# Performance work log

Measured on AMD Instinct MI355X. Metric: run time of the kernel, lower is better.

The kernel has to match this reference:

```python
import jax, jax.numpy as jnp
import numpy as np

DIM_DICT = 64
SIZE_DICT = 512
TEMPERATURE = 0.5
EPS_GUMBEL = 1e-10
EPS_NORM = 1e-12
EPS_PPL = 1e-7


def _l2_normalize(x, axis):
    # torch F.normalize: x / max(||x||, eps)
    n = jnp.sqrt(jnp.sum(x * x, axis=axis, keepdims=True))
    return x / jnp.maximum(n, EPS_NORM)


def setup_inputs() -> dict:
    key = jax.random.key(0)
    k1, k2, k3 = jax.random.split(key, 3)
    bs, seq_len, d = 8, 1024, 512
    z = jax.random.normal(k1, (bs, seq_len, d), dtype=jnp.float32)
    codebook = jax.random.normal(k2, (SIZE_DICT, DIM_DICT), dtype=jnp.float32)
    n_flat = bs * seq_len * (d // DIM_DICT)
    gumbel_u = jax.random.uniform(k3, (n_flat, SIZE_DICT), dtype=jnp.float32)
    kappa_q = jnp.float32(1.0)
    return {"z_from_encoder": z, "kappa_q": kappa_q, "codebook": codebook,
            "gumbel_u": gumbel_u}


def reference(z_from_encoder, kappa_q, codebook, gumbel_u):
    bs, seq_len, d = z_from_encoder.shape
    # [bs, seq, groups, dim_dict], L2-normalized along dim_dict
    z_perm = z_from_encoder.reshape(bs, seq_len, -1, DIM_DICT)
    z_norm = _l2_normalize(z_perm, axis=3)
    cb_norm = _l2_normalize(codebook, axis=1)  # [K, dim]

    # logit = -distance = kappa_q * <z, c>   -> [N, K]
    z_flat = z_norm.reshape(-1, DIM_DICT)
    logit = kappa_q * jnp.matmul(z_flat, cb_norm.T)

    log_probabilities = jax.nn.log_softmax(logit, axis=-1)
    probabilities = jnp.exp(log_probabilities)

    # gumbel-softmax sample (train path)
    g = -jnp.log(-jnp.log(gumbel_u + EPS_GUMBEL) + EPS_GUMBEL)
    encodings = jax.nn.softmax((logit + g) / TEMPERATURE, axis=-1)

    z_quantized = jnp.matmul(encodings, cb_norm).reshape(z_perm.shape)
    z_to_decoder = z_quantized.reshape(bs, seq_len, -1)

    avg_probs = jnp.mean(jax.lax.stop_gradient(probabilities), axis=0)  # [K]

    kld_discrete = jnp.sum(probabilities * log_probabilities) / bs
    kld_continuous = jnp.mean(
        jnp.sum(z_from_encoder * (z_from_encoder - z_to_decoder) * kappa_q,
                axis=(1, 2)))
    loss = kld_discrete + kld_continuous
    perplexity = jnp.exp(-jnp.sum(avg_probs * jnp.log(avg_probs + EPS_PPL)))
    return z_to_decoder, loss, perplexity
```

## Files before the change

### kernel.cpp

```cpp
#include <hip/hip_runtime.h>
#include <cstdint>
#include <cstddef>


typedef __attribute__((ext_vector_type(8))) short short8;
typedef __attribute__((ext_vector_type(4))) float f32x4;

namespace {
constexpr float kEpsG = 1e-10f;
constexpr float kEpsN = 1e-12f;
constexpr float kEpsP = 1e-7f;
constexpr float kLog2e = 1.4426950408889634f;
constexpr float kLn2 = 0.6931471805599453f;
constexpr int kSlots = 128;
constexpr int kStride = 520;
constexpr int kOffCbn = 0;
constexpr int kOffCbt = 65536;
constexpr int kOffAvg = 131072;
constexpr int kOffCS  = 139264;
constexpr int kOffAcx = 140800;
constexpr int kLdsBytes = 157184;
}

__device__ __forceinline__ float wsum64(float v) {
#pragma unroll
    for (int m = 1; m < 64; m <<= 1) v += __shfl_xor(v, m, 64);
    return v;
}
__device__ __forceinline__ uint32_t pk_bf16(float a, float b) {
    uint32_t ua = __float_as_uint(a), ub = __float_as_uint(b);
    ua += 0x7fffu + ((ua >> 16) & 1u);
    ub += 0x7fffu + ((ub >> 16) & 1u);
    return (ua >> 16) | (ub & 0xffff0000u);
}
__device__ __forceinline__ uint16_t bf16_rne(float a) {
    uint32_t ua = __float_as_uint(a);
    ua += 0x7fffu + ((ua >> 16) & 1u);
    return (uint16_t)(ua >> 16);
}
__device__ __forceinline__ float dot4(float4 v) {
    return v.x * v.x + v.y * v.y + v.z * v.z + v.w * v.w;
}

__global__ __launch_bounds__(256) void k_prep(const float* __restrict__ cb,
                                              uint16_t* __restrict__ cbN,
                                              uint16_t* __restrict__ cbNT) {
    const int row = blockIdx.x * 4 + (threadIdx.x >> 6);
    const int lane = threadIdx.x & 63;
    const float v = cb[row * 64 + lane];
    const float ss = wsum64(v * v);
    const float nv = v / fmaxf(sqrtf(ss), kEpsN);
    const uint16_t h = bf16_rne(nv);
    cbN[row * 64 + lane] = h;
    cbNT[lane * 512 + row] = h;
}

__global__ __launch_bounds__(512, 2) void k_main(
    const float* __restrict__ z, const float* __restrict__ kqp,
    const float* __restrict__ gum, const uint16_t* __restrict__ cbN,
    const uint16_t* __restrict__ cbNT, float* __restrict__ out,
    float* __restrict__ g_part) {
    extern __shared__ float4 smem_al[];
    char* smem = (char*)smem_al;
    float* avg4 = (float*)(smem + kOffAvg);
    float (*cS)[2][16]  = (float(*)[2][16])(smem + kOffCS);
    float (*cW)[2][16]  = (float(*)[2][16])(smem + kOffCS + 512);
    float (*cS2)[2][16] = (float(*)[2][16])(smem + kOffCS + 1024);
    float4 (*accx)[2][2][64] = (float4(*)[2][2][64])(smem + kOffAcx);

    const int tid = threadIdx.x;
    const int wv = tid >> 6;
    const int tp = wv >> 1;
    const int W = wv & 1;
    const int l = tid & 63;
    const int g = l >> 4;
    const int rh = l & 15;
    const int r0 = blockIdx.x * 64 + tp * 16;
    const int row = r0 + rh;
    const float kq = *kqp;

#pragma unroll
    for (int it = 0; it < 16; ++it) {
        const int i = tid + 512 * it;
        const uint4 v = ((const uint4*)cbN)[i];
        const int r = i >> 3, c = i & 7;
        *(uint4*)(smem + r * 128 + (((c ^ (r & 7))) << 4)) = v;
    }
#pragma unroll
    for (int it = 0; it < 8; ++it) {
        const int i = tid + 512 * it;
        const uint4 v = ((const uint4*)cbNT)[i];
        const int d = i >> 6, c = i & 63;
        *(uint4*)(smem + kOffCbt + d * 1024 + ((c ^ (d & 7)) << 4)) = v;
    }

    const float* zr = z + (size_t)row * 64;
    const float4 a0 = *(const float4*)(zr + 8 * g);
    const float4 a1 = *(const float4*)(zr + 8 * g + 4);
    const float4 a2 = *(const float4*)(zr + 32 + 8 * g);
    const float4 a3 = *(const float4*)(zr + 36 + 8 * g);
    float ss = dot4(a0) + dot4(a1) + dot4(a2) + dot4(a3);
    ss += __shfl_xor(ss, 16, 64);
    ss += __shfl_xor(ss, 32, 64);
    const float scz = kq * kLog2e / fmaxf(sqrtf(ss), kEpsN);
    union U8 { short8 s; uint32_t u[4]; };
    U8 zb0, zb1;
    zb0.u[0] = pk_bf16(a0.x * scz, a0.y * scz);
    zb0.u[1] = pk_bf16(a0.z * scz, a0.w * scz);
    zb0.u[2] = pk_bf16(a1.x * scz, a1.y * scz);
    zb0.u[3] = pk_bf16(a1.z * scz, a1.w * scz);
    zb1.u[0] = pk_bf16(a2.x * scz, a2.y * scz);
    zb1.u[1] = pk_bf16(a2.z * scz, a2.w * scz);
    zb1.u[2] = pk_bf16(a3.x * scz, a3.y * scz);
    zb1.u[3] = pk_bf16(a3.z * scz, a3.w * scz);

    const float B1 = kq * kLog2e;

    const float* ur = gum + (size_t)row * 512 + 256 * W;
    float4 uN[4][4];
#pragma unroll
    for (int t = 0; t < 4; ++t)
#pragma unroll
        for (int j = 0; j < 4; ++j)
            uN[t][j] = *(const float4*)(ur + 64 * t + 16 * j + 4 * g);

    __syncthreads();

    uint32_t epk[32];
    float S4[4] = {0.f, 0.f, 0.f, 0.f}, W4[4] = {0.f, 0.f, 0.f, 0.f};
#pragma unroll
    for (int T = 0; T < 4; ++T) {
#pragma unroll
        for (int q = 0; q < 4; ++q) {
            const int R = 256 * W + 64 * T + 16 * q + rh;
            const char* rb = smem + R * 128;
            const short8 ca0 = *(const short8*)(rb + ((g ^ (R & 7)) << 4));
            const short8 ca1 = *(const short8*)(rb + (((g + 4) ^ (R & 7)) << 4));
            f32x4 acc = {0.f, 0.f, 0.f, 0.f};
            acc = __builtin_amdgcn_mfma_f32_16x16x32_bf16(ca0, zb0.s, acc, 0, 0, 0);
            acc = __builtin_amdgcn_mfma_f32_16x16x32_bf16(ca1, zb1.s, acc, 0, 0, 0);
            float e4[4];
#pragma unroll
            for (int i = 0; i < 4; ++i) {
                const float d = acc[i] - B1;
                const float e = __builtin_amdgcn_exp2f(d);
                e4[i] = e;
                S4[i] += e;
                W4[i] = fmaf(d, e, W4[i]);
            }
            epk[8 * T + 2 * q] = pk_bf16(e4[0], e4[1]);
            epk[8 * T + 2 * q + 1] = pk_bf16(e4[2], e4[3]);
        }
    }
    float Sr = (S4[0] + S4[1]) + (S4[2] + S4[3]);
    float Wr = (W4[0] + W4[1]) + (W4[2] + W4[3]);
    Sr += __shfl_xor(Sr, 16, 64);
    Sr += __shfl_xor(Sr, 32, 64);
    Wr += __shfl_xor(Wr, 16, 64);
    Wr += __shfl_xor(Wr, 32, 64);
    if (g == 0) { cS[tp][W][rh] = Sr; cW[tp][W][rh] = Wr; }
    __syncthreads();
    const float St = cS[tp][0][rh] + cS[tp][1][rh];
    const float Wt = cW[tp][0][rh] + cW[tp][1][rh];
    const float inv = 1.0f / St;
    const float kldd = kLn2 * (Wt * inv - __builtin_amdgcn_logf(St));

    float S24[4] = {0.f, 0.f, 0.f, 0.f};
    f32x4 acc2[4];
#pragma unroll
    for (int dt = 0; dt < 4; ++dt) acc2[dt] = (f32x4){0.f, 0.f, 0.f, 0.f};
    const int srcA = rh + 16 * ((2 * g) & 3);
    const int srcB = rh + 16 * ((2 * g + 1) & 3);
    const bool hi = (g & 2) != 0;

#pragma unroll
    for (int T = 0; T < 4; ++T) {
        float ev[16];
#pragma unroll
        for (int k2 = 0; k2 < 8; ++k2) {
            const uint32_t pe = epk[8 * T + k2];
            ev[2 * k2] = __uint_as_float(pe << 16);
            ev[2 * k2 + 1] = __uint_as_float(pe & 0xffff0000u);
        }

        float pf[8];
#pragma unroll
        for (int q = 0; q < 4; ++q) {
            const float uu[4] = {uN[T][q].x, uN[T][q].y, uN[T][q].z, uN[T][q].w};
            float e2v[4];
#pragma unroll
            for (int i = 0; i < 4; ++i) {
                const float lg = __builtin_amdgcn_logf(uu[i] + kEpsG);
                const float inr = fmaf(lg, -kLn2, kEpsG);
                const float r = __builtin_amdgcn_rcpf(inr);
                const float t = ev[4 * q + i] * r;
                const float e2 = t * t;
                e2v[i] = e2;
                S24[i] += e2;
            }
            pf[2 * q] = __uint_as_float(pk_bf16(e2v[0], e2v[1]));
            pf[2 * q + 1] = __uint_as_float(pk_bf16(e2v[2], e2v[3]));
        }

#pragma unroll
        for (int j = 0; j < 16; ++j) ev[j] *= inv;
#pragma unroll
        for (int m = 1, nv = 8; m <= 8; m <<= 1, nv >>= 1) {
            const bool up_ = (rh & m) != 0;
#pragma unroll
            for (int t = 0; t < nv; ++t) {
                const float a = ev[t], b = ev[t + nv];
                const float keep = up_ ? b : a;
                const float send = up_ ? a : b;
                ev[t] = keep + __shfl_xor(send, m, 64);
            }
        }
        const int jr = ((rh & 1) << 3) | ((rh & 2) << 1) | ((rh & 4) >> 1) |
                       ((rh & 8) >> 3);
        avg4[tp * 512 + 256 * W + 64 * T + 16 * (jr >> 2) + 4 * g + (jr & 3)] =
            ev[0];

#pragma unroll
        for (int ks = 0; ks < 2; ++ks) {
            const float a0lo = __shfl(pf[4 * ks + 0], srcA, 64);
            const float a1lo = __shfl(pf[4 * ks + 1], srcA, 64);
            const float a0hi = __shfl(pf[4 * ks + 2], srcA, 64);
            const float a1hi = __shfl(pf[4 * ks + 3], srcA, 64);
            const float b0lo = __shfl(pf[4 * ks + 0], srcB, 64);
            const float b1lo = __shfl(pf[4 * ks + 1], srcB, 64);
            const float b0hi = __shfl(pf[4 * ks + 2], srcB, 64);
            const float b1hi = __shfl(pf[4 * ks + 3], srcB, 64);
            U8 af;
            af.u[0] = __float_as_uint(hi ? a0hi : a0lo);
            af.u[1] = __float_as_uint(hi ? a1hi : a1lo);
            af.u[2] = __float_as_uint(hi ? b0hi : b0lo);
            af.u[3] = __float_as_uint(hi ? b1hi : b1lo);
#pragma unroll
            for (int dt = 0; dt < 4; ++dt) {
                const int D = rh + 16 * dt;
                const int c = 32 * W + 8 * T + 4 * ks + g;
                const short8 bf = *(const short8*)(smem + kOffCbt + D * 1024 +
                                                   ((c ^ (D & 7)) << 4));
                acc2[dt] = __builtin_amdgcn_mfma_f32_16x16x32_bf16(
                    af.s, bf, acc2[dt], 0, 0, 0);
            }
        }
    }

    float S2r = (S24[0] + S24[1]) + (S24[2] + S24[3]);
    S2r += __shfl_xor(S2r, 16, 64);
    S2r += __shfl_xor(S2r, 32, 64);
    if (g == 0) cS2[tp][W][rh] = S2r;
    if (W == 0) {
        accx[tp][0][0][l] = make_float4(acc2[2][0], acc2[2][1], acc2[2][2], acc2[2][3]);
        accx[tp][0][1][l] = make_float4(acc2[3][0], acc2[3][1], acc2[3][2], acc2[3][3]);
    } else {
        accx[tp][1][0][l] = make_float4(acc2[0][0], acc2[0][1], acc2[0][2], acc2[0][3]);
        accx[tp][1][1][l] = make_float4(acc2[1][0], acc2[1][1], acc2[1][2], acc2[1][3]);
    }
    __syncthreads();
    const float inv2 = 1.0f / (cS2[tp][0][rh] + cS2[tp][1][rh]);
    float ivi[4];
#pragma unroll
    for (int i = 0; i < 4; ++i) ivi[i] = __shfl(inv2, 4 * g + i, 64);

    float kldc = 0.f;
#define EPI(OV, XV, DT)                                                       \
    {                                                                         \
        const float oq[4] = {OV[0] + XV.x, OV[1] + XV.y, OV[2] + XV.z,        \
                             OV[3] + XV.w};                                   \
        _Pragma("unroll") for (int i = 0; i < 4; ++i) {                       \
            const float q = oq[i] * ivi[i];                                   \
            const size_t oi = (size_t)(r0 + 4 * g + i) * 64 + rh + 16 * (DT); \
            out[oi] = q;                                                      \
            const float zv = z[oi];                                           \
            kldc = fmaf(zv, zv - q, kldc);                                    \
        }                                                                     \
    }
    if (W == 0) {
        const float4 x0 = accx[tp][1][0][l];
        const float4 x1 = accx[tp][1][1][l];
        EPI(acc2[0], x0, 0)
        EPI(acc2[1], x1, 1)
    } else {
        const float4 x0 = accx[tp][0][0][l];
        const float4 x1 = accx[tp][0][1][l];
        EPI(acc2[2], x0, 2)
        EPI(acc2[3], x1, 3)
    }

    const int slot = blockIdx.x & (kSlots - 1);
    float* gp = g_part + (size_t)slot * kStride;
    const float kc = wsum64(kldc) * kq;
    const float kd = wsum64(kldd) * 0.25f;
    if (l == 0) {
        atomicAdd(&gp[513], kc);
        if (W == 0) atomicAdd(&gp[512], kd);
    }
    const float av = avg4[tid] + avg4[512 + tid] + avg4[1024 + tid] +
                     avg4[1536 + tid];
    atomicAdd(&gp[tid], av);
}

__global__ __launch_bounds__(512) void k_final(const float* __restrict__ g_part,
                                               float* __restrict__ out) {
    __shared__ float red[8];
    const int tid = threadIdx.x;
    float sacc = 0.f;
#pragma unroll 8
    for (int i = 0; i < kSlots; ++i) sacc += g_part[(size_t)i * kStride + tid];
    const float avg = sacc * (1.0f / 65536.0f);
    const float t = avg * __logf(avg + kEpsP);
    const float sw = wsum64(t);
    if ((tid & 63) == 0) red[tid >> 6] = sw;
    __syncthreads();
    if (tid == 0) {
        float tot = 0.f;
#pragma unroll
        for (int i = 0; i < 8; ++i) tot += red[i];
        float sc0 = 0.f, sc1 = 0.f;
        for (int i = 0; i < kSlots; ++i) {
            sc0 += g_part[(size_t)i * kStride + 512];
            sc1 += g_part[(size_t)i * kStride + 513];
        }
        out[4194304] = (sc0 + sc1) * 0.125f;
        out[4194305] = __expf(-tot);
    }
}

extern "C" void kernel_launch(void* const* d_in, const int* in_sizes, int n_in,
                              void* d_out, int out_size, void* d_ws, size_t ws_size,
                              hipStream_t stream) {
    (void)in_sizes; (void)n_in; (void)out_size; (void)ws_size;
    const float* z   = (const float*)d_in[0];
    const float* kq  = (const float*)d_in[1];
    const float* cb  = (const float*)d_in[2];
    const float* gum = (const float*)d_in[3];
    float* out = (float*)d_out;

    uint16_t* cbN  = (uint16_t*)d_ws;
    uint16_t* cbNT = cbN + 32768;
    float* g_part  = (float*)(cbNT + 32768);

    (void)hipFuncSetAttribute((const void*)k_main,
                              hipFuncAttributeMaxDynamicSharedMemorySize,
                              kLdsBytes);
    (void)hipMemsetAsync(g_part, 0, kSlots * kStride * sizeof(float), stream);
    k_prep<<<128, 256, 0, stream>>>(cb, cbN, cbNT);
    k_main<<<1024, 512, kLdsBytes, stream>>>(z, kq, gum, cbN, cbNT, out, g_part);
    k_final<<<1, 512, 0, stream>>>(g_part, out);
}
```

Measured before the change: 86.63 us.

## Fuse gumbel softmax and second matmul into logit tile loop with double-buffered loads

The gumbel-weighted exponentials and the encodings×codebook MFMA accumulation move into the same per-tile loop that computes the logits, so they no longer wait for a separate second pass. The uniform-noise loads now use two four-float4 buffers that are refilled two tiles ahead, replacing one 16-register array. This should cut register pressure and let global loads and transcendental math overlap with MFMA work. It relies on the unnormalized exp (e, not e/St) feeding the gumbel weights, which the original already did, and it keeps the averaging pass separate.

```diff
diff --git a/kernel.cpp b/kernel.cpp
--- a/kernel.cpp
+++ b/kernel.cpp
@@ -14,7 +14,6 @@
 constexpr float kLn2 = 0.6931471805599453f;
 constexpr int kSlots = 128;
 constexpr int kStride = 520;
-constexpr int kOffCbn = 0;
 constexpr int kOffCbt = 65536;
 constexpr int kOffAvg = 131072;
 constexpr int kOffCS  = 139264;
@@ -117,41 +116,95 @@
     const float B1 = kq * kLog2e;
 
     const float* ur = gum + (size_t)row * 512 + 256 * W;
-    float4 uN[4][4];
-#pragma unroll
-    for (int t = 0; t < 4; ++t)
-#pragma unroll
-        for (int j = 0; j < 4; ++j)
-            uN[t][j] = *(const float4*)(ur + 64 * t + 16 * j + 4 * g);
+    float4 uA[4], uB[4];
+#pragma unroll
+    for (int j = 0; j < 4; ++j) uA[j] = *(const float4*)(ur + 16 * j + 4 * g);
+#pragma unroll
+    for (int j = 0; j < 4; ++j)
+        uB[j] = *(const float4*)(ur + 64 + 16 * j + 4 * g);
 
     __syncthreads();
 
     uint32_t epk[32];
     float S4[4] = {0.f, 0.f, 0.f, 0.f}, W4[4] = {0.f, 0.f, 0.f, 0.f};
-#pragma unroll
-    for (int T = 0; T < 4; ++T) {
-#pragma unroll
-        for (int q = 0; q < 4; ++q) {
-            const int R = 256 * W + 64 * T + 16 * q + rh;
-            const char* rb = smem + R * 128;
-            const short8 ca0 = *(const short8*)(rb + ((g ^ (R & 7)) << 4));
-            const short8 ca1 = *(const short8*)(rb + (((g + 4) ^ (R & 7)) << 4));
-            f32x4 acc = {0.f, 0.f, 0.f, 0.f};
-            acc = __builtin_amdgcn_mfma_f32_16x16x32_bf16(ca0, zb0.s, acc, 0, 0, 0);
-            acc = __builtin_amdgcn_mfma_f32_16x16x32_bf16(ca1, zb1.s, acc, 0, 0, 0);
-            float e4[4];
-#pragma unroll
-            for (int i = 0; i < 4; ++i) {
-                const float d = acc[i] - B1;
-                const float e = __builtin_amdgcn_exp2f(d);
-                e4[i] = e;
-                S4[i] += e;
-                W4[i] = fmaf(d, e, W4[i]);
-            }
-            epk[8 * T + 2 * q] = pk_bf16(e4[0], e4[1]);
-            epk[8 * T + 2 * q + 1] = pk_bf16(e4[2], e4[3]);
-        }
-    }
+    float S24[4] = {0.f, 0.f, 0.f, 0.f};
+    f32x4 acc2[4];
+#pragma unroll
+    for (int dt = 0; dt < 4; ++dt) acc2[dt] = (f32x4){0.f, 0.f, 0.f, 0.f};
+    const int srcA = rh + 16 * ((2 * g) & 3);
+    const int srcB = rh + 16 * ((2 * g + 1) & 3);
+    const bool hi = (g & 2) != 0;
+
+#define RELOAD(UB, RT)                                                       \
+    _Pragma("unroll") for (int j = 0; j < 4; ++j)                            \
+        UB[j] = *(const float4*)(ur + 64 * (RT) + 16 * j + 4 * g);
+
+#define FTILE(T, UBUF, PRE)                                                  \
+    {                                                                        \
+        float pf[8];                                                         \
+        _Pragma("unroll") for (int q = 0; q < 4; ++q) {                      \
+            const int R = 256 * W + 64 * (T) + 16 * q + rh;                  \
+            const char* rb = smem + R * 128;                                 \
+            const short8 ca0 = *(const short8*)(rb + ((g ^ (R & 7)) << 4));  \
+            const short8 ca1 =                                               \
+                *(const short8*)(rb + (((g + 4) ^ (R & 7)) << 4));           \
+            f32x4 acc = {0.f, 0.f, 0.f, 0.f};                                \
+            acc = __builtin_amdgcn_mfma_f32_16x16x32_bf16(ca0, zb0.s, acc,   \
+                                                          0, 0, 0);          \
+            acc = __builtin_amdgcn_mfma_f32_16x16x32_bf16(ca1, zb1.s, acc,   \
+                                                          0, 0, 0);          \
+            const float uu[4] = {UBUF[q].x, UBUF[q].y, UBUF[q].z, UBUF[q].w};\
+            float e4[4], e2v[4];                                             \
+            _Pragma("unroll") for (int i = 0; i < 4; ++i) {                  \
+                const float d = acc[i] - B1;                                 \
+                const float e = __builtin_amdgcn_exp2f(d);                   \
+                e4[i] = e;                                                   \
+                S4[i] += e;                                                  \
+                W4[i] = fmaf(d, e, W4[i]);                                   \
+                const float lg = __builtin_amdgcn_logf(uu[i] + kEpsG);       \
+                const float inr = fmaf(lg, -kLn2, kEpsG);                    \
+                const float r = __builtin_amdgcn_rcpf(inr);                  \
+                const float t = e * r;                                       \
+                const float e2 = t * t;                                      \
+                e2v[i] = e2;                                                 \
+                S24[i] += e2;                                                \
+            }                                                                \
+            epk[8 * (T) + 2 * q] = pk_bf16(e4[0], e4[1]);                    \
+            epk[8 * (T) + 2 * q + 1] = pk_bf16(e4[2], e4[3]);                \
+            pf[2 * q] = __uint_as_float(pk_bf16(e2v[0], e2v[1]));            \
+            pf[2 * q + 1] = __uint_as_float(pk_bf16(e2v[2], e2v[3]));        \
+        }                                                                    \
+        PRE                                                                  \
+        _Pragma("unroll") for (int ks = 0; ks < 2; ++ks) {                   \
+            const float a0lo = __shfl(pf[4 * ks + 0], srcA, 64);             \
+            const float a1lo = __shfl(pf[4 * ks + 1], srcA, 64);             \
+            const float a0hi = __shfl(pf[4 * ks + 2], srcA, 64);             \
+            const float a1hi = __shfl(pf[4 * ks + 3], srcA, 64);             \
+            const float b0lo = __shfl(pf[4 * ks + 0], srcB, 64);             \
+            const float b1lo = __shfl(pf[4 * ks + 1], srcB, 64);             \
+            const float b0hi = __shfl(pf[4 * ks + 2], srcB, 64);             \
+            const float b1hi = __shfl(pf[4 * ks + 3], srcB, 64);             \
+            U8 af;                                                           \
+            af.u[0] = __float_as_uint(hi ? a0hi : a0lo);                     \
+            af.u[1] = __float_as_uint(hi ? a1hi : a1lo);                     \
+            af.u[2] = __float_as_uint(hi ? b0hi : b0lo);                     \
+            af.u[3] = __float_as_uint(hi ? b1hi : b1lo);                     \
+            _Pragma("unroll") for (int dt = 0; dt < 4; ++dt) {               \
+                const int D = rh + 16 * dt;                                  \
+                const int c = 32 * W + 8 * (T) + 4 * ks + g;                 \
+                const short8 bf = *(const short8*)(smem + kOffCbt +          \
+                    D * 1024 + ((c ^ (D & 7)) << 4));                        \
+                acc2[dt] = __builtin_amdgcn_mfma_f32_16x16x32_bf16(          \
+                    af.s, bf, acc2[dt], 0, 0, 0);                            \
+            }                                                                \
+        }                                                                    \
+    }
+
+    FTILE(0, uA, RELOAD(uA, 2))
+    FTILE(1, uB, RELOAD(uB, 3))
+    FTILE(2, uA, ;)
+    FTILE(3, uB, ;)
+
     float Sr = (S4[0] + S4[1]) + (S4[2] + S4[3]);
     float Wr = (W4[0] + W4[1]) + (W4[2] + W4[3]);
     Sr += __shfl_xor(Sr, 16, 64);
@@ -165,14 +218,6 @@
     const float inv = 1.0f / St;
     const float kldd = kLn2 * (Wt * inv - __builtin_amdgcn_logf(St));
 
-    float S24[4] = {0.f, 0.f, 0.f, 0.f};
-    f32x4 acc2[4];
-#pragma unroll
-    for (int dt = 0; dt < 4; ++dt) acc2[dt] = (f32x4){0.f, 0.f, 0.f, 0.f};
-    const int srcA = rh + 16 * ((2 * g) & 3);
-    const int srcB = rh + 16 * ((2 * g + 1) & 3);
-    const bool hi = (g & 2) != 0;
-
 #pragma unroll
     for (int T = 0; T < 4; ++T) {
         float ev[16];
@@ -182,26 +227,6 @@
             ev[2 * k2] = __uint_as_float(pe << 16);
             ev[2 * k2 + 1] = __uint_as_float(pe & 0xffff0000u);
         }
-
-        float pf[8];
-#pragma unroll
-        for (int q = 0; q < 4; ++q) {
-            const float uu[4] = {uN[T][q].x, uN[T][q].y, uN[T][q].z, uN[T][q].w};
-            float e2v[4];
-#pragma unroll
-            for (int i = 0; i < 4; ++i) {
-                const float lg = __builtin_amdgcn_logf(uu[i] + kEpsG);
-                const float inr = fmaf(lg, -kLn2, kEpsG);
-                const float r = __builtin_amdgcn_rcpf(inr);
-                const float t = ev[4 * q + i] * r;
-                const float e2 = t * t;
-                e2v[i] = e2;
-                S24[i] += e2;
-            }
-            pf[2 * q] = __uint_as_float(pk_bf16(e2v[0], e2v[1]));
-            pf[2 * q + 1] = __uint_as_float(pk_bf16(e2v[2], e2v[3]));
-        }
-
 #pragma unroll
         for (int j = 0; j < 16; ++j) ev[j] *= inv;
 #pragma unroll
@@ -219,32 +244,6 @@
                        ((rh & 8) >> 3);
         avg4[tp * 512 + 256 * W + 64 * T + 16 * (jr >> 2) + 4 * g + (jr & 3)] =
             ev[0];
-
-#pragma unroll
-        for (int ks = 0; ks < 2; ++ks) {
-            const float a0lo = __shfl(pf[4 * ks + 0], srcA, 64);
-            const float a1lo = __shfl(pf[4 * ks + 1], srcA, 64);
-            const float a0hi = __shfl(pf[4 * ks + 2], srcA, 64);
-            const float a1hi = __shfl(pf[4 * ks + 3], srcA, 64);
-            const float b0lo = __shfl(pf[4 * ks + 0], srcB, 64);
-            const float b1lo = __shfl(pf[4 * ks + 1], srcB, 64);
-            const float b0hi = __shfl(pf[4 * ks + 2], srcB, 64);
-            const float b1hi = __shfl(pf[4 * ks + 3], srcB, 64);
-            U8 af;
-            af.u[0] = __float_as_uint(hi ? a0hi : a0lo);
-            af.u[1] = __float_as_uint(hi ? a1hi : a1lo);
-            af.u[2] = __float_as_uint(hi ? b0hi : b0lo);
-            af.u[3] = __float_as_uint(hi ? b1hi : b1lo);
-#pragma unroll
-            for (int dt = 0; dt < 4; ++dt) {
-                const int D = rh + 16 * dt;
-                const int c = 32 * W + 8 * T + 4 * ks + g;
-                const short8 bf = *(const short8*)(smem + kOffCbt + D * 1024 +
-                                                   ((c ^ (D & 7)) << 4));
-                acc2[dt] = __builtin_amdgcn_mfma_f32_16x16x32_bf16(
-                    af.s, bf, acc2[dt], 0, 0, 0);
-            }
-        }
     }
 
     float S2r = (S24[0] + S24[1]) + (S24[2] + S24[3]);
```

Measured after the change: 84.76 us. 1.02x faster.

## Use 1024-thread blocks, recompute logits to drop stored exponentials, LDS atomic avg

Applied to the files above, without the earlier changes.

Each block now covers 128 rows with 1024 threads, so the 128 KB codebook LDS fill is amortized over twice as many rows and half as many blocks load it. The first pass fuses the Gumbel sample computation with the logit exponentials instead of holding packed exp values and prefetched uniforms in registers. A second MFMA pass recomputes the logits to accumulate normalized probabilities into the average vector, which now uses LDS atomics instead of per-tile arrays. This cuts register pressure at the cost of doubled matmul/exp work, extra barriers, and LDS atomic contention.

```diff
diff --git a/kernel.cpp b/kernel.cpp
--- a/kernel.cpp
+++ b/kernel.cpp
@@ -14,12 +14,11 @@
 constexpr float kLn2 = 0.6931471805599453f;
 constexpr int kSlots = 128;
 constexpr int kStride = 520;
-constexpr int kOffCbn = 0;
 constexpr int kOffCbt = 65536;
 constexpr int kOffAvg = 131072;
-constexpr int kOffCS  = 139264;
-constexpr int kOffAcx = 140800;
-constexpr int kLdsBytes = 157184;
+constexpr int kOffCS  = 133120;
+constexpr int kOffAcx = 136192;
+constexpr int kLdsBytes = 152576;
 }
 
 __device__ __forceinline__ float wsum64(float v) {
@@ -55,18 +54,18 @@
     cbNT[lane * 512 + row] = h;
 }
 
-__global__ __launch_bounds__(512, 2) void k_main(
+__global__ __launch_bounds__(1024, 4) void k_main(
     const float* __restrict__ z, const float* __restrict__ kqp,
     const float* __restrict__ gum, const uint16_t* __restrict__ cbN,
     const uint16_t* __restrict__ cbNT, float* __restrict__ out,
     float* __restrict__ g_part) {
     extern __shared__ float4 smem_al[];
     char* smem = (char*)smem_al;
-    float* avg4 = (float*)(smem + kOffAvg);
+    float* avg1 = (float*)(smem + kOffAvg);
     float (*cS)[2][16]  = (float(*)[2][16])(smem + kOffCS);
-    float (*cW)[2][16]  = (float(*)[2][16])(smem + kOffCS + 512);
-    float (*cS2)[2][16] = (float(*)[2][16])(smem + kOffCS + 1024);
-    float4 (*accx)[2][2][64] = (float4(*)[2][2][64])(smem + kOffAcx);
+    float (*cW)[2][16]  = (float(*)[2][16])(smem + kOffCS + 1024);
+    float (*cS2)[2][16] = (float(*)[2][16])(smem + kOffCS + 2048);
+    float4 (*accx)[2][64] = (float4(*)[2][64])(smem + kOffAcx);
 
     const int tid = threadIdx.x;
     const int wv = tid >> 6;
@@ -75,20 +74,21 @@
     const int l = tid & 63;
     const int g = l >> 4;
     const int rh = l & 15;
-    const int r0 = blockIdx.x * 64 + tp * 16;
+    const int r0 = blockIdx.x * 128 + tp * 16;
     const int row = r0 + rh;
     const float kq = *kqp;
 
-#pragma unroll
-    for (int it = 0; it < 16; ++it) {
-        const int i = tid + 512 * it;
+    if (tid < 512) avg1[tid] = 0.f;
+#pragma unroll
+    for (int it = 0; it < 8; ++it) {
+        const int i = tid + 1024 * it;
         const uint4 v = ((const uint4*)cbN)[i];
         const int r = i >> 3, c = i & 7;
-        *(uint4*)(smem + r * 128 + (((c ^ (r & 7))) << 4)) = v;
-    }
-#pragma unroll
-    for (int it = 0; it < 8; ++it) {
-        const int i = tid + 512 * it;
+        *(uint4*)(smem + r * 128 + ((c ^ (r & 7)) << 4)) = v;
+    }
+#pragma unroll
+    for (int it = 0; it < 4; ++it) {
+        const int i = tid + 1024 * it;
         const uint4 v = ((const uint4*)cbNT)[i];
         const int d = i >> 6, c = i & 63;
         *(uint4*)(smem + kOffCbt + d * 1024 + ((c ^ (d & 7)) << 4)) = v;
@@ -115,21 +115,27 @@
     zb1.u[3] = pk_bf16(a3.z * scz, a3.w * scz);
 
     const float B1 = kq * kLog2e;
-
     const float* ur = gum + (size_t)row * 512 + 256 * W;
-    float4 uN[4][4];
-#pragma unroll
-    for (int t = 0; t < 4; ++t)
+
+    __syncthreads();
+
+    float S4[4] = {0.f, 0.f, 0.f, 0.f}, W4[4] = {0.f, 0.f, 0.f, 0.f};
+    float S24[4] = {0.f, 0.f, 0.f, 0.f};
+    f32x4 acc2[4];
+#pragma unroll
+    for (int dt = 0; dt < 4; ++dt) acc2[dt] = (f32x4){0.f, 0.f, 0.f, 0.f};
+    const int srcA = rh + 16 * ((2 * g) & 3);
+    const int srcB = rh + 16 * ((2 * g + 1) & 3);
+    const bool hi = (g & 2) != 0;
+
+#pragma unroll
+    for (int T = 0; T < 4; ++T) {
+        float4 u4[4];
 #pragma unroll
         for (int j = 0; j < 4; ++j)
-            uN[t][j] = *(const float4*)(ur + 64 * t + 16 * j + 4 * g);
-
-    __syncthreads();
-
-    uint32_t epk[32];
-    float S4[4] = {0.f, 0.f, 0.f, 0.f}, W4[4] = {0.f, 0.f, 0.f, 0.f};
-#pragma unroll
-    for (int T = 0; T < 4; ++T) {
+            u4[j] = *(const float4*)(ur + 64 * T + 16 * j + 4 * g);
+
+        float pf[8];
 #pragma unroll
         for (int q = 0; q < 4; ++q) {
             const int R = 256 * W + 64 * T + 16 * q + rh;
@@ -139,61 +145,18 @@
             f32x4 acc = {0.f, 0.f, 0.f, 0.f};
             acc = __builtin_amdgcn_mfma_f32_16x16x32_bf16(ca0, zb0.s, acc, 0, 0, 0);
             acc = __builtin_amdgcn_mfma_f32_16x16x32_bf16(ca1, zb1.s, acc, 0, 0, 0);
-            float e4[4];
+            const float uu[4] = {u4[q].x, u4[q].y, u4[q].z, u4[q].w};
+            float e2v[4];
 #pragma unroll
             for (int i = 0; i < 4; ++i) {
                 const float d = acc[i] - B1;
                 const float e = __builtin_amdgcn_exp2f(d);
-                e4[i] = e;
                 S4[i] += e;
                 W4[i] = fmaf(d, e, W4[i]);
-            }
-            epk[8 * T + 2 * q] = pk_bf16(e4[0], e4[1]);
-            epk[8 * T + 2 * q + 1] = pk_bf16(e4[2], e4[3]);
-        }
-    }
-    float Sr = (S4[0] + S4[1]) + (S4[2] + S4[3]);
-    float Wr = (W4[0] + W4[1]) + (W4[2] + W4[3]);
-    Sr += __shfl_xor(Sr, 16, 64);
-    Sr += __shfl_xor(Sr, 32, 64);
-    Wr += __shfl_xor(Wr, 16, 64);
-    Wr += __shfl_xor(Wr, 32, 64);
-    if (g == 0) { cS[tp][W][rh] = Sr; cW[tp][W][rh] = Wr; }
-    __syncthreads();
-    const float St = cS[tp][0][rh] + cS[tp][1][rh];
-    const float Wt = cW[tp][0][rh] + cW[tp][1][rh];
-    const float inv = 1.0f / St;
-    const float kldd = kLn2 * (Wt * inv - __builtin_amdgcn_logf(St));
-
-    float S24[4] = {0.f, 0.f, 0.f, 0.f};
-    f32x4 acc2[4];
-#pragma unroll
-    for (int dt = 0; dt < 4; ++dt) acc2[dt] = (f32x4){0.f, 0.f, 0.f, 0.f};
-    const int srcA = rh + 16 * ((2 * g) & 3);
-    const int srcB = rh + 16 * ((2 * g + 1) & 3);
-    const bool hi = (g & 2) != 0;
-
-#pragma unroll
-    for (int T = 0; T < 4; ++T) {
-        float ev[16];
-#pragma unroll
-        for (int k2 = 0; k2 < 8; ++k2) {
-            const uint32_t pe = epk[8 * T + k2];
-            ev[2 * k2] = __uint_as_float(pe << 16);
-            ev[2 * k2 + 1] = __uint_as_float(pe & 0xffff0000u);
-        }
-
-        float pf[8];
-#pragma unroll
-        for (int q = 0; q < 4; ++q) {
-            const float uu[4] = {uN[T][q].x, uN[T][q].y, uN[T][q].z, uN[T][q].w};
-            float e2v[4];
-#pragma unroll
-            for (int i = 0; i < 4; ++i) {
                 const float lg = __builtin_amdgcn_logf(uu[i] + kEpsG);
                 const float inr = fmaf(lg, -kLn2, kEpsG);
                 const float r = __builtin_amdgcn_rcpf(inr);
-                const float t = ev[4 * q + i] * r;
+                const float t = e * r;
                 const float e2 = t * t;
                 e2v[i] = e2;
                 S24[i] += e2;
@@ -201,25 +164,6 @@
             pf[2 * q] = __uint_as_float(pk_bf16(e2v[0], e2v[1]));
             pf[2 * q + 1] = __uint_as_float(pk_bf16(e2v[2], e2v[3]));
         }
-
-#pragma unroll
-        for (int j = 0; j < 16; ++j) ev[j] *= inv;
-#pragma unroll
-        for (int m = 1, nv = 8; m <= 8; m <<= 1, nv >>= 1) {
-            const bool up_ = (rh & m) != 0;
-#pragma unroll
-            for (int t = 0; t < nv; ++t) {
-                const float a = ev[t], b = ev[t + nv];
-                const float keep = up_ ? b : a;
-                const float send = up_ ? a : b;
-                ev[t] = keep + __shfl_xor(send, m, 64);
-            }
-        }
-        const int jr = ((rh & 1) << 3) | ((rh & 2) << 1) | ((rh & 4) >> 1) |
-                       ((rh & 8) >> 3);
-        avg4[tp * 512 + 256 * W + 64 * T + 16 * (jr >> 2) + 4 * g + (jr & 3)] =
-            ev[0];
-
 #pragma unroll
         for (int ks = 0; ks < 2; ++ks) {
             const float a0lo = __shfl(pf[4 * ks + 0], srcA, 64);
@@ -247,22 +191,74 @@
         }
     }
 
+    float Sr = (S4[0] + S4[1]) + (S4[2] + S4[3]);
+    float Wr = (W4[0] + W4[1]) + (W4[2] + W4[3]);
+    Sr += __shfl_xor(Sr, 16, 64);
+    Sr += __shfl_xor(Sr, 32, 64);
+    Wr += __shfl_xor(Wr, 16, 64);
+    Wr += __shfl_xor(Wr, 32, 64);
+    if (g == 0) { cS[tp][W][rh] = Sr; cW[tp][W][rh] = Wr; }
+    __syncthreads();
+    const float St = cS[tp][0][rh] + cS[tp][1][rh];
+    const float Wt = cW[tp][0][rh] + cW[tp][1][rh];
+    const float inv = 1.0f / St;
+    const float kldd = kLn2 * (Wt * inv - __builtin_amdgcn_logf(St));
+
+#pragma unroll
+    for (int T = 0; T < 4; ++T) {
+        float ev[16];
+#pragma unroll
+        for (int q = 0; q < 4; ++q) {
+            const int R = 256 * W + 64 * T + 16 * q + rh;
+            const char* rb = smem + R * 128;
+            const short8 ca0 = *(const short8*)(rb + ((g ^ (R & 7)) << 4));
+            const short8 ca1 = *(const short8*)(rb + (((g + 4) ^ (R & 7)) << 4));
+            f32x4 acc = {0.f, 0.f, 0.f, 0.f};
+            acc = __builtin_amdgcn_mfma_f32_16x16x32_bf16(ca0, zb0.s, acc, 0, 0, 0);
+            acc = __builtin_amdgcn_mfma_f32_16x16x32_bf16(ca1, zb1.s, acc, 0, 0, 0);
+#pragma unroll
+            for (int i = 0; i < 4; ++i)
+                ev[4 * q + i] = __builtin_amdgcn_exp2f(acc[i] - B1) * inv;
+        }
+#pragma unroll
+        for (int m = 1, nv = 8; m <= 8; m <<= 1, nv >>= 1) {
+            const bool up_ = (rh & m) != 0;
+#pragma unroll
+            for (int t = 0; t < nv; ++t) {
+                const float a = ev[t], b = ev[t + nv];
+                const float keep = up_ ? b : a;
+                const float send = up_ ? a : b;
+                ev[t] = keep + __shfl_xor(send, m, 64);
+            }
+        }
+        const int jr = ((rh & 1) << 3) | ((rh & 2) << 1) | ((rh & 4) >> 1) |
+                       ((rh & 8) >> 3);
+        atomicAdd(&avg1[256 * W + 64 * T + 16 * (jr >> 2) + 4 * g + (jr & 3)],
+                  ev[0]);
+    }
+
     float S2r = (S24[0] + S24[1]) + (S24[2] + S24[3]);
     S2r += __shfl_xor(S2r, 16, 64);
     S2r += __shfl_xor(S2r, 32, 64);
     if (g == 0) cS2[tp][W][rh] = S2r;
     if (W == 0) {
-        accx[tp][0][0][l] = make_float4(acc2[2][0], acc2[2][1], acc2[2][2], acc2[2][3]);
-        accx[tp][0][1][l] = make_float4(acc2[3][0], acc2[3][1], acc2[3][2], acc2[3][3]);
-    } else {
-        accx[tp][1][0][l] = make_float4(acc2[0][0], acc2[0][1], acc2[0][2], acc2[0][3]);
-        accx[tp][1][1][l] = make_float4(acc2[1][0], acc2[1][1], acc2[1][2], acc2[1][3]);
+        accx[tp][0][l] = make_float4(acc2[2][0], acc2[2][1], acc2[2][2], acc2[2][3]);
+        accx[tp][1][l] = make_float4(acc2[3][0], acc2[3][1], acc2[3][2], acc2[3][3]);
     }
     __syncthreads();
     const float inv2 = 1.0f / (cS2[tp][0][rh] + cS2[tp][1][rh]);
     float ivi[4];
 #pragma unroll
     for (int i = 0; i < 4; ++i) ivi[i] = __shfl(inv2, 4 * g + i, 64);
+    float4 x0, x1;
+    if (W == 1) { x0 = accx[tp][0][l]; x1 = accx[tp][1][l]; }
+    __syncthreads();
+    if (W == 1) {
+        accx[tp][0][l] = make_float4(acc2[0][0], acc2[0][1], acc2[0][2], acc2[0][3]);
+        accx[tp][1][l] = make_float4(acc2[1][0], acc2[1][1], acc2[1][2], acc2[1][3]);
+    }
+    __syncthreads();
+    if (W == 0) { x0 = accx[tp][0][l]; x1 = accx[tp][1][l]; }
 
     float kldc = 0.f;
 #define EPI(OV, XV, DT)                                                       \
@@ -278,13 +274,9 @@
         }                                                                     \
     }
     if (W == 0) {
-        const float4 x0 = accx[tp][1][0][l];
-        const float4 x1 = accx[tp][1][1][l];
         EPI(acc2[0], x0, 0)
         EPI(acc2[1], x1, 1)
     } else {
-        const float4 x0 = accx[tp][0][0][l];
-        const float4 x1 = accx[tp][0][1][l];
         EPI(acc2[2], x0, 2)
         EPI(acc2[3], x1, 3)
     }
@@ -297,9 +289,8 @@
         atomicAdd(&gp[513], kc);
         if (W == 0) atomicAdd(&gp[512], kd);
     }
-    const float av = avg4[tid] + avg4[512 + tid] + avg4[1024 + tid] +
-                     avg4[1536 + tid];
-    atomicAdd(&gp[tid], av);
+    __syncthreads();
+    if (tid < 512) atomicAdd(&gp[tid], avg1[tid]);
 }
 
 __global__ __launch_bounds__(512) void k_final(const float* __restrict__ g_part,
@@ -347,6 +338,6 @@
                               kLdsBytes);
     (void)hipMemsetAsync(g_part, 0, kSlots * kStride * sizeof(float), stream);
     k_prep<<<128, 256, 0, stream>>>(cb, cbN, cbNT);
-    k_main<<<1024, 512, kLdsBytes, stream>>>(z, kq, gum, cbN, cbNT, out, g_part);
+    k_main<<<512, 1024, kLdsBytes, stream>>>(z, kq, gum, cbN, cbNT, out, g_part);
     k_final<<<1, 512, 0, stream>>>(g_part, out);
 }
```

Result: no change. 85.79 us (-1.0%).

## Fuse gumbel softmax and second MFMA into logit loop with streamed LDS gumbel tiles

Applied to the files above, without the earlier changes.

Moves the gumbel-noise transform and the encodings×codebook MFMA into the first logit loop, so each 16-column quartet is consumed as soon as it is produced. Gumbel uniforms are no longer held as 64 registers per thread. They are loaded with coalesced row-wise float4 loads, staged per wave in swizzled LDS, and double-buffered so the next tile's load overlaps compute. The launch-bounds occupancy hint of 2 is removed, which relaxes register limits and may change occupancy. The LDS layout is compacted to reuse space for the staging buffers. A dead QUARTET macro is left defined then undefined.

```diff
diff --git a/kernel.cpp b/kernel.cpp
--- a/kernel.cpp
+++ b/kernel.cpp
@@ -14,11 +14,9 @@
 constexpr float kLn2 = 0.6931471805599453f;
 constexpr int kSlots = 128;
 constexpr int kStride = 520;
-constexpr int kOffCbn = 0;
 constexpr int kOffCbt = 65536;
-constexpr int kOffAvg = 131072;
-constexpr int kOffCS  = 139264;
-constexpr int kOffAcx = 140800;
+constexpr int kOffCS  = 131072;
+constexpr int kOffU   = 132608;
 constexpr int kLdsBytes = 157184;
 }
 
@@ -55,18 +53,18 @@
     cbNT[lane * 512 + row] = h;
 }
 
-__global__ __launch_bounds__(512, 2) void k_main(
+__global__ __launch_bounds__(512) void k_main(
     const float* __restrict__ z, const float* __restrict__ kqp,
     const float* __restrict__ gum, const uint16_t* __restrict__ cbN,
     const uint16_t* __restrict__ cbNT, float* __restrict__ out,
     float* __restrict__ g_part) {
     extern __shared__ float4 smem_al[];
     char* smem = (char*)smem_al;
-    float* avg4 = (float*)(smem + kOffAvg);
     float (*cS)[2][16]  = (float(*)[2][16])(smem + kOffCS);
     float (*cW)[2][16]  = (float(*)[2][16])(smem + kOffCS + 512);
     float (*cS2)[2][16] = (float(*)[2][16])(smem + kOffCS + 1024);
-    float4 (*accx)[2][2][64] = (float4(*)[2][2][64])(smem + kOffAcx);
+    float* avg4 = (float*)(smem + kOffU);
+    float4 (*accx)[2][2][64] = (float4(*)[2][2][64])(smem + kOffU + 8192);
 
     const int tid = threadIdx.x;
     const int wv = tid >> 6;
@@ -78,6 +76,8 @@
     const int r0 = blockIdx.x * 64 + tp * 16;
     const int row = r0 + rh;
     const float kq = *kqp;
+
+    float4* us16 = (float4*)(smem + kOffU + wv * 2048);
 
 #pragma unroll
     for (int it = 0; it < 16; ++it) {
@@ -116,42 +116,146 @@
 
     const float B1 = kq * kLog2e;
 
-    const float* ur = gum + (size_t)row * 512 + 256 * W;
-    float4 uN[4][4];
-#pragma unroll
-    for (int t = 0; t < 4; ++t)
-#pragma unroll
-        for (int j = 0; j < 4; ++j)
-            uN[t][j] = *(const float4*)(ur + 64 * t + 16 * j + 4 * g);
+    const int srow0 = l >> 3;
+    const int scol = l & 7;
+    const float* gbase = gum + (size_t)r0 * 512 + 256 * W + scol * 4;
+#define LOADU(S0, S1, T, H)                                                  \
+    {                                                                        \
+        const float* p = gbase + 64 * (T) + 32 * (H);                        \
+        S0 = *(const float4*)(p + (size_t)(srow0)*512);                      \
+        S1 = *(const float4*)(p + (size_t)(srow0 + 8) * 512);                \
+    }
+#define WRITEU(S0, S1)                                                       \
+    {                                                                        \
+        us16[srow0 * 8 + (scol ^ (srow0 & 7))] = S0;                         \
+        us16[(srow0 + 8) * 8 + (scol ^ ((srow0 + 8) & 7))] = S1;             \
+    }
+
+    float4 s0, s1;
+    LOADU(s0, s1, 0, 0)
 
     __syncthreads();
 
     uint32_t epk[32];
     float S4[4] = {0.f, 0.f, 0.f, 0.f}, W4[4] = {0.f, 0.f, 0.f, 0.f};
-#pragma unroll
-    for (int T = 0; T < 4; ++T) {
-#pragma unroll
-        for (int q = 0; q < 4; ++q) {
-            const int R = 256 * W + 64 * T + 16 * q + rh;
-            const char* rb = smem + R * 128;
-            const short8 ca0 = *(const short8*)(rb + ((g ^ (R & 7)) << 4));
-            const short8 ca1 = *(const short8*)(rb + (((g + 4) ^ (R & 7)) << 4));
-            f32x4 acc = {0.f, 0.f, 0.f, 0.f};
-            acc = __builtin_amdgcn_mfma_f32_16x16x32_bf16(ca0, zb0.s, acc, 0, 0, 0);
-            acc = __builtin_amdgcn_mfma_f32_16x16x32_bf16(ca1, zb1.s, acc, 0, 0, 0);
-            float e4[4];
-#pragma unroll
-            for (int i = 0; i < 4; ++i) {
-                const float d = acc[i] - B1;
-                const float e = __builtin_amdgcn_exp2f(d);
-                e4[i] = e;
-                S4[i] += e;
-                W4[i] = fmaf(d, e, W4[i]);
-            }
-            epk[8 * T + 2 * q] = pk_bf16(e4[0], e4[1]);
-            epk[8 * T + 2 * q + 1] = pk_bf16(e4[2], e4[3]);
-        }
-    }
+    float S24[4] = {0.f, 0.f, 0.f, 0.f};
+    f32x4 acc2[4];
+#pragma unroll
+    for (int dt = 0; dt < 4; ++dt) acc2[dt] = (f32x4){0.f, 0.f, 0.f, 0.f};
+    const int srcA = rh + 16 * ((2 * g) & 3);
+    const int srcB = rh + 16 * ((2 * g + 1) & 3);
+    const bool hi = (g & 2) != 0;
+
+#define QUARTET(T, Q, PF)                                                    \
+    {                                                                        \
+        const int R = 256 * W + 64 * (T) + 16 * (Q) + rh;                    \
+        const char* rb = smem + R * 128;                                     \
+        const short8 ca0 = *(const short8*)(rb + ((g ^ (R & 7)) << 4));      \
+        const short8 ca1 = *(const short8*)(rb + (((g + 4) ^ (R & 7)) << 4));\
+        f32x4 acc = {0.f, 0.f, 0.f, 0.f};                                    \
+        acc = __builtin_amdgcn_mfma_f32_16x16x32_bf16(ca0, zb0.s, acc, 0, 0, 0); \
+        acc = __builtin_amdgcn_mfma_f32_16x16x32_bf16(ca1, zb1.s, acc, 0, 0, 0); \
+        const float4 uq = us16[rh * 8 + (((((Q)&1) * 4) + g) ^ (rh & 7))];   \
+        const float uu[4] = {uq.x, uq.y, uq.z, uq.w};                        \
+        float e4[4], e2v[4];                                                 \
+        _Pragma("unroll") for (int i = 0; i < 4; ++i) {                      \
+            const float d = acc[i] - B1;                                     \
+            const float e = __builtin_amdgcn_exp2f(d);                       \
+            e4[i] = e;                                                       \
+            S4[i] += e;                                                      \
+            W4[i] = fmaf(d, e, W4[i]);                                       \
+            const float lg = __builtin_amdgcn_logf(uu[i] + kEpsG);           \
+            const float inr = fmaf(lg, -kLn2, kEpsG);                        \
+            const float r = __builtin_amdgcn_rcpf(inr);                      \
+            const float t = e * r;                                           \
+            const float e2 = t * t;                                          \
+            e2v[i] = e2;                                                     \
+            S24[i] += e2;                                                    \
+        }                                                                    \
+        epk[8 * (T) + 2 * (Q)] = pk_bf16(e4[0], e4[1]);                      \
+        epk[8 * (T) + 2 * (Q) + 1] = pk_bf16(e4[2], e4[3]);                  \
+        PF[2 * (Q)&3 ? 0 : 0] = PF[0];       \
+        PF[((Q)&1) * 2 + 0 + (((Q) >> 31) & 0)] = PF[((Q)&1) * 2];           \
+    }
+#undef QUARTET
+
+#define QRT(T, Q, P0, P1)                                                    \
+    {                                                                        \
+        const int R = 256 * W + 64 * (T) + 16 * (Q) + rh;                    \
+        const char* rb = smem + R * 128;                                     \
+        const short8 ca0 = *(const short8*)(rb + ((g ^ (R & 7)) << 4));      \
+        const short8 ca1 = *(const short8*)(rb + (((g + 4) ^ (R & 7)) << 4));\
+        f32x4 acc = {0.f, 0.f, 0.f, 0.f};                                    \
+        acc = __builtin_amdgcn_mfma_f32_16x16x32_bf16(ca0, zb0.s, acc, 0, 0, 0); \
+        acc = __builtin_amdgcn_mfma_f32_16x16x32_bf16(ca1, zb1.s, acc, 0, 0, 0); \
+        const float4 uq = us16[rh * 8 + ((((Q & 1) * 4) + g) ^ (rh & 7))];   \
+        const float uu[4] = {uq.x, uq.y, uq.z, uq.w};                        \
+        float e4[4], e2v[4];                                                 \
+        _Pragma("unroll") for (int i = 0; i < 4; ++i) {                      \
+            const float d = acc[i] - B1;                                     \
+            const float e = __builtin_amdgcn_exp2f(d);                       \
+            e4[i] = e;                                                       \
+            S4[i] += e;                                                      \
+            W4[i] = fmaf(d, e, W4[i]);                                       \
+            const float lg = __builtin_amdgcn_logf(uu[i] + kEpsG);           \
+            const float inr = fmaf(lg, -kLn2, kEpsG);                        \
+            const float r = __builtin_amdgcn_rcpf(inr);                      \
+            const float t = e * r;                                           \
+            const float e2 = t * t;                                          \
+            e2v[i] = e2;                                                     \
+            S24[i] += e2;                                                    \
+        }                                                                    \
+        epk[8 * (T) + 2 * (Q)] = pk_bf16(e4[0], e4[1]);                      \
+        epk[8 * (T) + 2 * (Q) + 1] = pk_bf16(e4[2], e4[3]);                  \
+        P0 = __uint_as_float(pk_bf16(e2v[0], e2v[1]));                       \
+        P1 = __uint_as_float(pk_bf16(e2v[2], e2v[3]));                       \
+    }
+
+#define EXCH(T, KS, PFA, PFB, PFC, PFD)                                      \
+    {                                                                        \
+        const float a0lo = __shfl(PFA, srcA, 64);                            \
+        const float a1lo = __shfl(PFB, srcA, 64);                            \
+        const float a0hi = __shfl(PFC, srcA, 64);                            \
+        const float a1hi = __shfl(PFD, srcA, 64);                            \
+        const float b0lo = __shfl(PFA, srcB, 64);                            \
+        const float b1lo = __shfl(PFB, srcB, 64);                            \
+        const float b0hi = __shfl(PFC, srcB, 64);                            \
+        const float b1hi = __shfl(PFD, srcB, 64);                            \
+        U8 af;                                                               \
+        af.u[0] = __float_as_uint(hi ? a0hi : a0lo);                         \
+        af.u[1] = __float_as_uint(hi ? a1hi : a1lo);                         \
+        af.u[2] = __float_as_uint(hi ? b0hi : b0lo);                         \
+        af.u[3] = __float_as_uint(hi ? b1hi : b1lo);                         \
+        _Pragma("unroll") for (int dt = 0; dt < 4; ++dt) {                   \
+            const int D = rh + 16 * dt;                                      \
+            const int c = 32 * W + 8 * (T) + 4 * (KS) + g;                   \
+            const short8 bf = *(const short8*)(smem + kOffCbt + D * 1024 +   \
+                                               ((c ^ (D & 7)) << 4));        \
+            acc2[dt] = __builtin_amdgcn_mfma_f32_16x16x32_bf16(              \
+                af.s, bf, acc2[dt], 0, 0, 0);                                \
+        }                                                                    \
+    }
+
+#define FTILE(T, LAST)                                                       \
+    {                                                                        \
+        float p0, p1, p2, p3;                                                \
+        WRITEU(s0, s1)                                    \
+        LOADU(s0, s1, T, 1)                                 \
+        QRT(T, 0, p0, p1)                                                    \
+        QRT(T, 1, p2, p3)                                                    \
+        EXCH(T, 0, p0, p1, p2, p3)                                           \
+        WRITEU(s0, s1)                       \
+        if (!(LAST)) LOADU(s0, s1, (T) + 1, 0)    \
+        QRT(T, 2, p0, p1)                                                    \
+        QRT(T, 3, p2, p3)                                                    \
+        EXCH(T, 1, p0, p1, p2, p3)                                           \
+    }
+
+    FTILE(0, 0)
+    FTILE(1, 0)
+    FTILE(2, 0)
+    FTILE(3, 1)
+
     float Sr = (S4[0] + S4[1]) + (S4[2] + S4[3]);
     float Wr = (W4[0] + W4[1]) + (W4[2] + W4[3]);
     Sr += __shfl_xor(Sr, 16, 64);
@@ -165,14 +269,6 @@
     const float inv = 1.0f / St;
     const float kldd = kLn2 * (Wt * inv - __builtin_amdgcn_logf(St));
 
-    float S24[4] = {0.f, 0.f, 0.f, 0.f};
-    f32x4 acc2[4];
-#pragma unroll
-    for (int dt = 0; dt < 4; ++dt) acc2[dt] = (f32x4){0.f, 0.f, 0.f, 0.f};
-    const int srcA = rh + 16 * ((2 * g) & 3);
-    const int srcB = rh + 16 * ((2 * g + 1) & 3);
-    const bool hi = (g & 2) != 0;
-
 #pragma unroll
     for (int T = 0; T < 4; ++T) {
         float ev[16];
@@ -182,26 +278,6 @@
             ev[2 * k2] = __uint_as_float(pe << 16);
             ev[2 * k2 + 1] = __uint_as_float(pe & 0xffff0000u);
         }
-
-        float pf[8];
-#pragma unroll
-        for (int q = 0; q < 4; ++q) {
-            const float uu[4] = {uN[T][q].x, uN[T][q].y, uN[T][q].z, uN[T][q].w};
-            float e2v[4];
-#pragma unroll
-            for (int i = 0; i < 4; ++i) {
-                const float lg = __builtin_amdgcn_logf(uu[i] + kEpsG);
-                const float inr = fmaf(lg, -kLn2, kEpsG);
-                const float r = __builtin_amdgcn_rcpf(inr);
-                const float t = ev[4 * q + i] * r;
-                const float e2 = t * t;
-                e2v[i] = e2;
-                S24[i] += e2;
-            }
-            pf[2 * q] = __uint_as_float(pk_bf16(e2v[0], e2v[1]));
-            pf[2 * q + 1] = __uint_as_float(pk_bf16(e2v[2], e2v[3]));
-        }
-
 #pragma unroll
         for (int j = 0; j < 16; ++j) ev[j] *= inv;
 #pragma unroll
@@ -219,32 +295,6 @@
                        ((rh & 8) >> 3);
         avg4[tp * 512 + 256 * W + 64 * T + 16 * (jr >> 2) + 4 * g + (jr & 3)] =
             ev[0];
-
-#pragma unroll
-        for (int ks = 0; ks < 2; ++ks) {
-            const float a0lo = __shfl(pf[4 * ks + 0], srcA, 64);
-            const float a1lo = __shfl(pf[4 * ks + 1], srcA, 64);
-            const float a0hi = __shfl(pf[4 * ks + 2], srcA, 64);
-            const float a1hi = __shfl(pf[4 * ks + 3], srcA, 64);
-            const float b0lo = __shfl(pf[4 * ks + 0], srcB, 64);
-            const float b1lo = __shfl(pf[4 * ks + 1], srcB, 64);
-            const float b0hi = __shfl(pf[4 * ks + 2], srcB, 64);
-            const float b1hi = __shfl(pf[4 * ks + 3], srcB, 64);
-            U8 af;
-            af.u[0] = __float_as_uint(hi ? a0hi : a0lo);
-            af.u[1] = __float_as_uint(hi ? a1hi : a1lo);
-            af.u[2] = __float_as_uint(hi ? b0hi : b0lo);
-            af.u[3] = __float_as_uint(hi ? b1hi : b1lo);
-#pragma unroll
-            for (int dt = 0; dt < 4; ++dt) {
-                const int D = rh + 16 * dt;
-                const int c = 32 * W + 8 * T + 4 * ks + g;
-                const short8 bf = *(const short8*)(smem + kOffCbt + D * 1024 +
-                                                   ((c ^ (D & 7)) << 4));
-                acc2[dt] = __builtin_amdgcn_mfma_f32_16x16x32_bf16(
-                    af.s, bf, acc2[dt], 0, 0, 0);
-            }
-        }
     }
 
     float S2r = (S24[0] + S24[1]) + (S24[2] + S24[3]);
```

Measured after the change: 86.86 us. About the same (+0.3%).
